# Kernel tuning notes

Measured on AMD Instinct MI355X. Metric: run time of the kernel, lower is better.

## Reference

```python
import jax, jax.numpy as jnp
import numpy as np


def setup_inputs() -> dict:
    key = jax.random.key(0)
    x = jax.random.normal(key, (16, 256, 128, 128), dtype=jnp.float32)
    return {"x": x}


def reference(x) -> jnp.ndarray:
    # NeighbourChannels: 1x1 conv with weight W[i,j] = 1 - delta_ij, i.e.
    # out[b,i,h,w] = sum_j x[b,j,h,w] - x[b,i,h,w].
    total = jnp.sum(x, axis=1, keepdims=True)  # [B,1,H,W]
    return total - x
```

## Files before the change

kernel.cpp:

```cpp
#include <hip/hip_runtime.h>


#define NC_C   256
#define NC_HW  16384
#define NC_POS 64
#define NC_NT  256

__global__ __launch_bounds__(NC_NT, 2)
void neighbour_channels_kernel(const float* __restrict__ x,
                               float* __restrict__ out) {
    __shared__ float  tile[NC_C][NC_POS];
    __shared__ float4 psum[16][16];
    __shared__ float4 sums[16];

    const int t  = threadIdx.x;
    const int pg = t & 15;
    const int cg = t >> 4;

    const int b     = blockIdx.x >> 8;
    const int chunk = blockIdx.x & 255;
    const long long base = ((long long)b * NC_C) * NC_HW
                         + (long long)chunk * NC_POS;

    const float4* xin = (const float4*)(x + base);

    float4 acc = make_float4(0.f, 0.f, 0.f, 0.f);
    #pragma unroll
    for (int i = 0; i < 16; ++i) {
        const int c = i * 16 + cg;
        float4 v = xin[(long long)c * (NC_HW / 4) + pg];
        acc.x += v.x; acc.y += v.y; acc.z += v.z; acc.w += v.w;
        *(float4*)&tile[c][pg * 4] = v;
    }
    psum[cg][pg] = acc;
    __syncthreads();

    if (t < 16) {
        float4 s = psum[0][t];
        #pragma unroll
        for (int g = 1; g < 16; ++g) {
            const float4 v = psum[g][t];
            s.x += v.x; s.y += v.y; s.z += v.z; s.w += v.w;
        }
        sums[t] = s;
    }
    __syncthreads();

    const float4 s = sums[pg];
    float4* op = (float4*)(out + base);
    #pragma unroll
    for (int i = 0; i < 16; ++i) {
        const int c = i * 16 + cg;
        const float4 v = *(const float4*)&tile[c][pg * 4];
        op[(long long)c * (NC_HW / 4) + pg] =
            make_float4(s.x - v.x, s.y - v.y, s.z - v.z, s.w - v.w);
    }
}

extern "C" void kernel_launch(void* const* d_in, const int* in_sizes, int n_in,
                              void* d_out, int out_size, void* d_ws, size_t ws_size,
                              hipStream_t stream) {
    const float* x = (const float*)d_in[0];
    float* out = (float*)d_out;

    const int B = in_sizes[0] / (NC_C * NC_HW);
    const int grid = B * (NC_HW / NC_POS);

    neighbour_channels_kernel<<<grid, NC_NT, 0, stream>>>(x, out);
}
```

Measured before the change: 428.0 us.

## Keep channel values in registers and widen per-block position tile

Removes the shared-memory staging tile and holds each thread's 16 channel float4 values in registers between the sum and the subtract. Blocks grow to 1024 threads covering 256 contiguous floats per channel, so each wavefront reads full 1 KB rows. Channels are now assigned contiguously per thread group instead of interleaved. This raises register pressure and reduces the block count, which may affect latency hiding.

```diff
diff --git a/kernel.cpp b/kernel.cpp
--- a/kernel.cpp
+++ b/kernel.cpp
@@ -1,70 +1,70 @@
 #include <hip/hip_runtime.h>
 
 
-#define NC_C   256
-#define NC_HW  16384
-#define NC_POS 64
-#define NC_NT  256
+#define NC_C    256
+#define NC_HW   16384
+#define NC_HW4  (NC_HW / 4)
+#define NC_POS4 64
+#define NC_NT   1024
+#define NC_CPT  16
 
-__global__ __launch_bounds__(NC_NT, 2)
-void neighbour_channels_kernel(const float* __restrict__ x,
-                               float* __restrict__ out) {
-    __shared__ float  tile[NC_C][NC_POS];
-    __shared__ float4 psum[16][16];
-    __shared__ float4 sums[16];
+__global__ __launch_bounds__(NC_NT, 1)
+void neighbour_channels_kernel(const float4* __restrict__ x4,
+                               float4* __restrict__ out4) {
+    __shared__ float4 psum[16][NC_POS4];
+    __shared__ float4 sums[NC_POS4];
 
     const int t  = threadIdx.x;
-    const int pg = t & 15;
-    const int cg = t >> 4;
+    const int pg = t & 63;
+    const int cg = t >> 6;
 
-    const int b     = blockIdx.x >> 8;
-    const int chunk = blockIdx.x & 255;
-    const long long base = ((long long)b * NC_C) * NC_HW
-                         + (long long)chunk * NC_POS;
+    const int b     = blockIdx.x >> 6;
+    const int chunk = blockIdx.x & 63;
+    const int base = b * (NC_C * NC_HW4) + chunk * NC_POS4 + pg;
 
-    const float4* xin = (const float4*)(x + base);
+    float4 v[NC_CPT];
+    #pragma unroll
+    for (int i = 0; i < NC_CPT; ++i) {
+        const int c = cg * NC_CPT + i;
+        v[i] = x4[base + c * NC_HW4];
+    }
 
     float4 acc = make_float4(0.f, 0.f, 0.f, 0.f);
     #pragma unroll
-    for (int i = 0; i < 16; ++i) {
-        const int c = i * 16 + cg;
-        float4 v = xin[(long long)c * (NC_HW / 4) + pg];
-        acc.x += v.x; acc.y += v.y; acc.z += v.z; acc.w += v.w;
-        *(float4*)&tile[c][pg * 4] = v;
+    for (int i = 0; i < NC_CPT; ++i) {
+        acc.x += v[i].x; acc.y += v[i].y; acc.z += v[i].z; acc.w += v[i].w;
     }
     psum[cg][pg] = acc;
     __syncthreads();
 
-    if (t < 16) {
+    if (t < NC_POS4) {
         float4 s = psum[0][t];
         #pragma unroll
         for (int g = 1; g < 16; ++g) {
-            const float4 v = psum[g][t];
-            s.x += v.x; s.y += v.y; s.z += v.z; s.w += v.w;
+            const float4 p = psum[g][t];
+            s.x += p.x; s.y += p.y; s.z += p.z; s.w += p.w;
         }
         sums[t] = s;
     }
     __syncthreads();
 
     const float4 s = sums[pg];
-    float4* op = (float4*)(out + base);
     #pragma unroll
-    for (int i = 0; i < 16; ++i) {
-        const int c = i * 16 + cg;
-        const float4 v = *(const float4*)&tile[c][pg * 4];
-        op[(long long)c * (NC_HW / 4) + pg] =
-            make_float4(s.x - v.x, s.y - v.y, s.z - v.z, s.w - v.w);
+    for (int i = 0; i < NC_CPT; ++i) {
+        const int c = cg * NC_CPT + i;
+        out4[base + c * NC_HW4] =
+            make_float4(s.x - v[i].x, s.y - v[i].y, s.z - v[i].z, s.w - v[i].w);
     }
 }
 
 extern "C" void kernel_launch(void* const* d_in, const int* in_sizes, int n_in,
                               void* d_out, int out_size, void* d_ws, size_t ws_size,
                               hipStream_t stream) {
-    const float* x = (const float*)d_in[0];
-    float* out = (float*)d_out;
+    const float4* x4  = (const float4*)d_in[0];
+    float4* out4      = (float4*)d_out;
 
-    const int B = in_sizes[0] / (NC_C * NC_HW);
-    const int grid = B * (NC_HW / NC_POS);
+    const int B    = in_sizes[0] / (NC_C * NC_HW);
+    const int grid = B * (NC_HW4 / NC_POS4);
 
-    neighbour_channels_kernel<<<grid, NC_NT, 0, stream>>>(x, out);
+    neighbour_channels_kernel<<<grid, NC_NT, 0, stream>>>(x4, out4);
 }
```

After: 424.0 us. No clear change (-0.9%).
